# Kernel optimization log

Measured on AMD Instinct MI355X. Metric: run time of the kernel, lower is better.

## Reference

```python
import jax, jax.numpy as jnp
import numpy as np

ALPHA = 0.5
BETA = 0.5


def _attend(qk, feat, W, wp, b):
    """One additive co-attention stage.
    qk:   (B, K)     projected query
    feat: (B, N, D)  keys/values
    W:    (D, K), wp: (2K, 1), b: (N,)
    returns (B, D) attention-weighted sum of feat.
    """
    proj = jnp.einsum('bnd,dk->bnk', feat, W)                    # (B,N,K)
    q = jnp.broadcast_to(qk[:, None, :], proj.shape)             # repeat query
    H = jnp.tanh(jnp.concatenate([q, proj], axis=-1))            # (B,N,2K)
    logits = jnp.einsum('bnk,k->bn', H, wp[:, 0]) + b            # (B,N)
    P = jax.nn.softmax(logits, axis=-1)
    return jnp.einsum('bn,bnd->bd', P, feat)                     # (B,D)


def setup_inputs() -> dict:
    key = jax.random.key(0)
    B, R, S, G, E, D, K = 256, 49, 128, 20, 30, 1024, 256
    ks = jax.random.split(key, 19)
    w = lambda k, shp: 0.05 * jax.random.normal(k, shp, jnp.float32)
    return {
        'ifeature_h': jax.random.normal(ks[0], (B, R, D), jnp.float32),
        'tfeature_h': jax.random.normal(ks[1], (B, S, D), jnp.float32),
        'cfeature':   jax.random.normal(ks[2], (B, G, D), jnp.float32),
        'efeature':   jax.random.normal(ks[3], (B, E, D), jnp.float32),
        'w_Vit_0':  w(ks[4],  (D, K)),
        'w_Vc_0':   w(ks[5],  (D, K)),
        'w_Pc_0':   w(ks[6],  (2 * K, 1)),
        'b_Pc_0':   jnp.zeros((G,), jnp.float32),
        'w_Ve_0':   w(ks[7],  (D, K)),
        'w_Pe_0':   w(ks[8],  (2 * K, 1)),
        'b_Pe_0':   jnp.zeros((E,), jnp.float32),
        'w_Vi_1':   w(ks[9],  (D, K)),
        'w_Vtce_1': w(ks[10], (D, K)),
        'w_Pi_1':   w(ks[11], (2 * K, 1)),
        'b_Pi_1':   jnp.zeros((R,), jnp.float32),
        'w_Vice_2': w(ks[12], (D, K)),
        'w_Vt_2':   w(ks[13], (D, K)),
        'w_Pt_2':   w(ks[14], (2 * K, 1)),
        'b_Pt_2':   jnp.zeros((S,), jnp.float32),
    }


def reference(ifeature_h, tfeature_h, cfeature, efeature,
              w_Vit_0, w_Vc_0, w_Pc_0, b_Pc_0,
              w_Ve_0, w_Pe_0, b_Pe_0,
              w_Vi_1, w_Vtce_1, w_Pi_1, b_Pi_1,
              w_Vice_2, w_Vt_2, w_Pt_2, b_Pt_2):
    ifeat = jnp.mean(ifeature_h, axis=1)   # (B, D)
    tfeat = jnp.mean(tfeature_h, axis=1)   # (B, D)

    # stage 0: image+text query attends over caption group and title
    q0 = (ifeat + tfeat) @ w_Vit_0                               # (B, K)
    Vc = _attend(q0, cfeature, w_Vc_0, w_Pc_0, b_Pc_0)           # (B, D)
    Ve = _attend(q0, efeature, w_Ve_0, w_Pe_0, b_Pe_0)           # (B, D)

    # stage 1: text+caption+title query attends over image regions
    q1 = (tfeat + ALPHA * Vc + BETA * Ve) @ w_Vtce_1
    Vi = _attend(q1, ifeature_h, w_Vi_1, w_Pi_1, b_Pi_1)

    # stage 2: image+caption+title query attends over text tokens
    q2 = (Vi + ALPHA * Vc + BETA * Ve) @ w_Vice_2
    Vt = _attend(q2, tfeature_h, w_Vt_2, w_Pt_2, b_Pt_2)

    return Vi + Vt + ALPHA * Vc + BETA * Ve
```

## Files before the change

kernel.cpp:

```cpp
#include <hip/hip_runtime.h>
#include <hip/hip_bf16.h>
#include <stdint.h>


#define D_DIM 1024
#define K_OUT 256
#define BM 128
#define BK 64
#define NT (D_DIM / BK)

typedef float f32x4 __attribute__((ext_vector_type(4)));
typedef short bf16x8 __attribute__((ext_vector_type(8)));
typedef unsigned short u16x8 __attribute__((ext_vector_type(8)));

static __device__ __forceinline__ unsigned short f2bf(float f) {
    return __builtin_bit_cast(unsigned short, __float2bfloat16(f));
}

static __device__ __forceinline__ float fast_tanh(float x) {
    float e = __expf(2.0f * x);
    return 1.0f - 2.0f / (e + 1.0f);
}

__global__ __launch_bounds__(256) void convert_wt(
    const float* __restrict__ w_c, const float* __restrict__ w_e,
    const float* __restrict__ w_i, const float* __restrict__ w_t,
    unsigned short* __restrict__ wt_all)
{
    const float* wsel[4] = {w_c, w_e, w_i, w_t};
    const float* W = wsel[blockIdx.x];
    unsigned short* Wt = wt_all + (size_t)blockIdx.x * (K_OUT * D_DIM);
    const int d0 = blockIdx.y * 32;

    __shared__ float tile[32][K_OUT];
    const int t = threadIdx.x;
    for (int i = 0; i < 32; ++i) {
        int idx = t + i * 256;
        int dd = idx >> 8, n = idx & 255;
        tile[dd][n] = W[(size_t)(d0 + dd) * K_OUT + n];
    }
    __syncthreads();
    unsigned short buf[32];
#pragma unroll
    for (int dd = 0; dd < 32; ++dd) buf[dd] = f2bf(tile[dd][t]);
#pragma unroll
    for (int i = 0; i < 4; ++i) {
        u16x8 v;
#pragma unroll
        for (int j = 0; j < 8; ++j) v[j] = buf[i * 8 + j];
        *reinterpret_cast<u16x8*>(&Wt[(size_t)t * D_DIM + d0 + i * 8]) = v;
    }
}

struct GemmStage {
    const float* feat;
    const unsigned short* wt;
    const float* wp;
    float* s_out;
    int blk_start;
};

__global__ __launch_bounds__(512) void logits_gemm(
    GemmStage g0, GemmStage g1, GemmStage g2, GemmStage g3)
{
    __shared__ __align__(16) unsigned char AsRaw[BM * 128];
    __shared__ __align__(16) unsigned char WsRaw[K_OUT * 128];
    __shared__ float wp2s[K_OUT];
    __shared__ float partial[BM][4];

    GemmStage st;
    const int bid = blockIdx.x;
    if (bid < g1.blk_start) st = g0;
    else if (bid < g2.blk_start) st = g1;
    else if (bid < g3.blk_start) st = g2;
    else st = g3;
    const int m0 = (bid - st.blk_start) * BM;

    const int t = threadIdx.x;
    if (t < K_OUT) wp2s[t] = st.wp[K_OUT + t];

    const int ar = t >> 2, ac2 = t & 3;
    const int wr = t >> 3, wc = t & 7;
    const int wv = t >> 6, lane = t & 63;
    const int wm = wv >> 2, wn = wv & 3;
    const int q = lane >> 4, c16 = lane & 15;
    const int xa = c16 & 7;

    f32x4 acc[4][4];
#pragma unroll
    for (int i = 0; i < 4; ++i)
#pragma unroll
        for (int j = 0; j < 4; ++j) acc[i][j] = (f32x4){0.f, 0.f, 0.f, 0.f};

    const float* aptr = st.feat + (size_t)(m0 + ar) * D_DIM + ac2 * 16;
    const unsigned short* wptr = st.wt + (size_t)wr * D_DIM + wc * 8;
    const int ab0 = ar * 128 + ((((ac2 * 2)    ) ^ (ar & 7)) << 4);
    const int ab1 = ar * 128 + ((((ac2 * 2) + 1) ^ (ar & 7)) << 4);
    const int wb0 = wr * 128 + ((wc ^ (wr & 7)) << 4);

    f32x4 pa[4];
    u16x8 pw[4];

#pragma unroll
    for (int j = 0; j < 4; ++j) pa[j] = *reinterpret_cast<const f32x4*>(aptr + j * 4);
#pragma unroll
    for (int i = 0; i < 4; ++i) pw[i] = *reinterpret_cast<const u16x8*>(wptr + (size_t)i * 64 * D_DIM);
    {
        u16x8 o0, o1;
#pragma unroll
        for (int j = 0; j < 4; ++j) {
            o0[j] = f2bf(pa[0][j]); o0[4 + j] = f2bf(pa[1][j]);
            o1[j] = f2bf(pa[2][j]); o1[4 + j] = f2bf(pa[3][j]);
        }
        *reinterpret_cast<u16x8*>(&AsRaw[ab0]) = o0;
        *reinterpret_cast<u16x8*>(&AsRaw[ab1]) = o1;
#pragma unroll
        for (int i = 0; i < 4; ++i)
            *reinterpret_cast<u16x8*>(&WsRaw[wb0 + i * 64 * 128]) = pw[i];
    }

#pragma unroll 1
    for (int kt = 0; kt < NT; ++kt) {
        if (kt + 1 < NT) {
            const int d1 = (kt + 1) * BK;
#pragma unroll
            for (int j = 0; j < 4; ++j)
                pa[j] = *reinterpret_cast<const f32x4*>(aptr + d1 + j * 4);
#pragma unroll
            for (int i = 0; i < 4; ++i)
                pw[i] = *reinterpret_cast<const u16x8*>(wptr + (size_t)i * 64 * D_DIM + d1);
        }
        __syncthreads();
#pragma unroll
        for (int ks = 0; ks < 2; ++ks) {
            bf16x8 af[4], bfr[4];
            const int ck = (((ks * 4 + q) ^ xa)) << 4;
#pragma unroll
            for (int mt = 0; mt < 4; ++mt) {
                const int row = wm * 64 + mt * 16 + c16;
                af[mt] = *reinterpret_cast<const bf16x8*>(&AsRaw[row * 128 + ck]);
            }
#pragma unroll
            for (int nt = 0; nt < 4; ++nt) {
                const int row = wn * 64 + nt * 16 + c16;
                bfr[nt] = *reinterpret_cast<const bf16x8*>(&WsRaw[row * 128 + ck]);
            }
#pragma unroll
            for (int mt = 0; mt < 4; ++mt)
#pragma unroll
                for (int nt = 0; nt < 4; ++nt)
                    acc[mt][nt] = __builtin_amdgcn_mfma_f32_16x16x32_bf16(
                        af[mt], bfr[nt], acc[mt][nt], 0, 0, 0);
        }
        __syncthreads();
        if (kt + 1 < NT) {
            u16x8 o0, o1;
#pragma unroll
            for (int j = 0; j < 4; ++j) {
                o0[j] = f2bf(pa[0][j]); o0[4 + j] = f2bf(pa[1][j]);
                o1[j] = f2bf(pa[2][j]); o1[4 + j] = f2bf(pa[3][j]);
            }
            *reinterpret_cast<u16x8*>(&AsRaw[ab0]) = o0;
            *reinterpret_cast<u16x8*>(&AsRaw[ab1]) = o1;
#pragma unroll
            for (int i = 0; i < 4; ++i)
                *reinterpret_cast<u16x8*>(&WsRaw[wb0 + i * 64 * 128]) = pw[i];
        }
    }

#pragma unroll
    for (int mt = 0; mt < 4; ++mt) {
#pragma unroll
        for (int r = 0; r < 4; ++r) {
            float v = 0.f;
#pragma unroll
            for (int nt = 0; nt < 4; ++nt) {
                const int col = wn * 64 + nt * 16 + c16;
                v += fast_tanh(acc[mt][nt][r]) * wp2s[col];
            }
            v += __shfl_xor(v, 1);
            v += __shfl_xor(v, 2);
            v += __shfl_xor(v, 4);
            v += __shfl_xor(v, 8);
            if (c16 == 0) partial[wm * 64 + mt * 16 + q * 4 + r][wn] = v;
        }
    }
    __syncthreads();
    if (t < BM)
        st.s_out[m0 + t] = partial[t][0] + partial[t][1] + partial[t][2] + partial[t][3];
}

struct PVStage {
    const float* s;
    const float* bias;
    const float* feat;
    float* v_out;
    int N;
};

__global__ __launch_bounds__(256) void softmax_pv(
    PVStage p0, PVStage p1, PVStage p2, PVStage p3)
{
    PVStage st = (blockIdx.y == 0) ? p0 : (blockIdx.y == 1) ? p1
               : (blockIdx.y == 2) ? p2 : p3;
    const int b = blockIdx.x, t = threadIdx.x;
    const int N = st.N;

    __shared__ float P[128];
    __shared__ float inv_s;

    if (t < N) P[t] = st.s[b * N + t] + st.bias[t];
    __syncthreads();
    if (t < 64) {
        float m = -3.4e38f;
        for (int n = t; n < N; n += 64) m = fmaxf(m, P[n]);
#pragma unroll
        for (int sh = 32; sh; sh >>= 1) m = fmaxf(m, __shfl_xor(m, sh));
        float ssum = 0.f;
        for (int n = t; n < N; n += 64) { float e = __expf(P[n] - m); P[n] = e; ssum += e; }
#pragma unroll
        for (int sh = 32; sh; sh >>= 1) ssum += __shfl_xor(ssum, sh);
        if (t == 0) inv_s = 1.0f / ssum;
    }
    __syncthreads();
    const float inv = inv_s;

    f32x4 accv = (f32x4){0.f, 0.f, 0.f, 0.f};
    const float* fb = st.feat + (size_t)b * N * D_DIM + t * 4;
    for (int n = 0; n < N; ++n) {
        f32x4 f = *reinterpret_cast<const f32x4*>(fb + (size_t)n * D_DIM);
        accv += (P[n] * inv) * f;
    }
    *reinterpret_cast<f32x4*>(&st.v_out[(size_t)b * D_DIM + t * 4]) = accv;
}

__global__ __launch_bounds__(256) void combine_out(
    const float* __restrict__ vc, const float* __restrict__ ve,
    const float* __restrict__ vi, const float* __restrict__ vt,
    float* __restrict__ out)
{
    const int i = (blockIdx.x * 256 + threadIdx.x) * 4;
    f32x4 a = *reinterpret_cast<const f32x4*>(vi + i);
    f32x4 bb = *reinterpret_cast<const f32x4*>(vt + i);
    f32x4 c = *reinterpret_cast<const f32x4*>(vc + i);
    f32x4 e = *reinterpret_cast<const f32x4*>(ve + i);
    *reinterpret_cast<f32x4*>(out + i) = a + bb + 0.5f * c + 0.5f * e;
}

extern "C" void kernel_launch(void* const* d_in, const int* in_sizes, int n_in,
                              void* d_out, int out_size, void* d_ws, size_t ws_size,
                              hipStream_t stream)
{
    const float* ifeature = (const float*)d_in[0];
    const float* tfeature = (const float*)d_in[1];
    const float* cfeature = (const float*)d_in[2];
    const float* efeature = (const float*)d_in[3];
    const float* w_Vc = (const float*)d_in[5];
    const float* w_Pc = (const float*)d_in[6];
    const float* b_Pc = (const float*)d_in[7];
    const float* w_Ve = (const float*)d_in[8];
    const float* w_Pe = (const float*)d_in[9];
    const float* b_Pe = (const float*)d_in[10];
    const float* w_Vi = (const float*)d_in[11];
    const float* w_Pi = (const float*)d_in[13];
    const float* b_Pi = (const float*)d_in[14];
    const float* w_Vt = (const float*)d_in[16];
    const float* w_Pt = (const float*)d_in[17];
    const float* b_Pt = (const float*)d_in[18];

    char* ws = (char*)d_ws;
    unsigned short* wt = (unsigned short*)ws;
    float* s_c = (float*)(ws + 2u * 1024 * 1024);
    float* s_e = s_c + 5120;
    float* s_i = s_e + 7680;
    float* s_t = s_i + 12544;
    float* v_c = (float*)(ws + 3u * 1024 * 1024);
    float* v_e = v_c + 256 * 1024;
    float* v_i = v_e + 256 * 1024;
    float* v_t = v_i + 256 * 1024;

    convert_wt<<<dim3(4, 32), 256, 0, stream>>>(w_Vc, w_Ve, w_Vi, w_Vt, wt);

    GemmStage g0{cfeature, wt + 0 * (K_OUT * D_DIM), w_Pc, s_c, 0};
    GemmStage g1{efeature, wt + 1 * (K_OUT * D_DIM), w_Pe, s_e, 40};
    GemmStage g2{ifeature, wt + 2 * (K_OUT * D_DIM), w_Pi, s_i, 100};
    GemmStage g3{tfeature, wt + 3 * (K_OUT * D_DIM), w_Pt, s_t, 198};
    logits_gemm<<<454, 512, 0, stream>>>(g0, g1, g2, g3);

    PVStage p0{s_c, b_Pc, cfeature, v_c, 20};
    PVStage p1{s_e, b_Pe, efeature, v_e, 30};
    PVStage p2{s_i, b_Pi, ifeature, v_i, 49};
    PVStage p3{s_t, b_Pt, tfeature, v_t, 128};
    softmax_pv<<<dim3(256, 4), 256, 0, stream>>>(p0, p1, p2, p3);

    combine_out<<<256, 256, 0, stream>>>(v_c, v_e, v_i, v_t, (float*)d_out);
}
```

Before: 113.4 us.

## Pre-swizzle bf16 weights into MFMA fragment layout and read B directly from global

```diff
diff --git a/kernel.cpp b/kernel.cpp
--- a/kernel.cpp
+++ b/kernel.cpp
@@ -5,9 +5,9 @@
 
 #define D_DIM 1024
 #define K_OUT 256
-#define BM 128
+#define BM 64
 #define BK 64
-#define NT (D_DIM / BK)
+#define NT 16
 
 typedef float f32x4 __attribute__((ext_vector_type(4)));
 typedef short bf16x8 __attribute__((ext_vector_type(8)));
@@ -25,31 +25,25 @@
 __global__ __launch_bounds__(256) void convert_wt(
     const float* __restrict__ w_c, const float* __restrict__ w_e,
     const float* __restrict__ w_i, const float* __restrict__ w_t,
-    unsigned short* __restrict__ wt_all)
+    unsigned short* __restrict__ wtf)
 {
     const float* wsel[4] = {w_c, w_e, w_i, w_t};
     const float* W = wsel[blockIdx.x];
-    unsigned short* Wt = wt_all + (size_t)blockIdx.x * (K_OUT * D_DIM);
-    const int d0 = blockIdx.y * 32;
-
-    __shared__ float tile[32][K_OUT];
+    unsigned short* out = wtf + (size_t)blockIdx.x * (K_OUT * D_DIM);
+    const int kb = blockIdx.y;
     const int t = threadIdx.x;
-    for (int i = 0; i < 32; ++i) {
-        int idx = t + i * 256;
-        int dd = idx >> 8, n = idx & 255;
-        tile[dd][n] = W[(size_t)(d0 + dd) * K_OUT + n];
-    }
-    __syncthreads();
-    unsigned short buf[32];
-#pragma unroll
-    for (int dd = 0; dd < 32; ++dd) buf[dd] = f2bf(tile[dd][t]);
-#pragma unroll
-    for (int i = 0; i < 4; ++i) {
-        u16x8 v;
-#pragma unroll
-        for (int j = 0; j < 8; ++j) v[j] = buf[i * 8 + j];
-        *reinterpret_cast<u16x8*>(&Wt[(size_t)t * D_DIM + d0 + i * 8]) = v;
-    }
+
+    unsigned short tmp[16];
+#pragma unroll
+    for (int j = 0; j < 16; ++j)
+        tmp[j] = f2bf(W[(size_t)(kb * 16 + j) * K_OUT + t]);
+
+    u16x8 lo, hi;
+#pragma unroll
+    for (int j = 0; j < 8; ++j) { lo[j] = tmp[j]; hi[j] = tmp[8 + j]; }
+    unsigned short* dst = out + (size_t)kb * 4096 + t * 16;
+    *reinterpret_cast<u16x8*>(dst) = lo;
+    *reinterpret_cast<u16x8*>(dst + 8) = hi;
 }
 
 struct GemmStage {
@@ -60,16 +54,14 @@
     int blk_start;
 };
 
-__global__ __launch_bounds__(512) void logits_gemm(
+__global__ __launch_bounds__(256, 3) void logits_gemm(
     GemmStage g0, GemmStage g1, GemmStage g2, GemmStage g3)
 {
-    __shared__ __align__(16) unsigned char AsRaw[BM * 128];
-    __shared__ __align__(16) unsigned char WsRaw[K_OUT * 128];
-    __shared__ float wp2s[K_OUT];
+    __shared__ __align__(16) unsigned char As[2][BM * 128];
     __shared__ float partial[BM][4];
 
+    const int bid = blockIdx.x;
     GemmStage st;
-    const int bid = blockIdx.x;
     if (bid < g1.blk_start) st = g0;
     else if (bid < g2.blk_start) st = g1;
     else if (bid < g3.blk_start) st = g2;
@@ -77,14 +69,21 @@
     const int m0 = (bid - st.blk_start) * BM;
 
     const int t = threadIdx.x;
-    if (t < K_OUT) wp2s[t] = st.wp[K_OUT + t];
-
-    const int ar = t >> 2, ac2 = t & 3;
-    const int wr = t >> 3, wc = t & 7;
+    const int r = t >> 2, qd = t & 3;
     const int wv = t >> 6, lane = t & 63;
-    const int wm = wv >> 2, wn = wv & 3;
     const int q = lane >> 4, c16 = lane & 15;
-    const int xa = c16 & 7;
+
+    const float* aptr = st.feat + (size_t)(m0 + r) * D_DIM + qd * 16;
+    const int wo0 = r * 128 + (((qd * 2    ) ^ (r & 7)) << 4);
+    const int wo1 = r * 128 + (((qd * 2 + 1) ^ (r & 7)) << 4);
+    const unsigned short* bb = st.wt + (q >> 1) * 4096
+                             + ((wv * 64 + c16) << 4) + (q & 1) * 8;
+    const int ck0 = ((0 * 4 + q) ^ (c16 & 7)) << 4;
+    const int ck1 = ((1 * 4 + q) ^ (c16 & 7)) << 4;
+
+    float wpf[4];
+#pragma unroll
+    for (int nt = 0; nt < 4; ++nt) wpf[nt] = st.wp[K_OUT + wv * 64 + nt * 16 + c16];
 
     f32x4 acc[4][4];
 #pragma unroll
@@ -92,19 +91,10 @@
 #pragma unroll
         for (int j = 0; j < 4; ++j) acc[i][j] = (f32x4){0.f, 0.f, 0.f, 0.f};
 
-    const float* aptr = st.feat + (size_t)(m0 + ar) * D_DIM + ac2 * 16;
-    const unsigned short* wptr = st.wt + (size_t)wr * D_DIM + wc * 8;
-    const int ab0 = ar * 128 + ((((ac2 * 2)    ) ^ (ar & 7)) << 4);
-    const int ab1 = ar * 128 + ((((ac2 * 2) + 1) ^ (ar & 7)) << 4);
-    const int wb0 = wr * 128 + ((wc ^ (wr & 7)) << 4);
-
     f32x4 pa[4];
-    u16x8 pw[4];
-
-#pragma unroll
-    for (int j = 0; j < 4; ++j) pa[j] = *reinterpret_cast<const f32x4*>(aptr + j * 4);
-#pragma unroll
-    for (int i = 0; i < 4; ++i) pw[i] = *reinterpret_cast<const u16x8*>(wptr + (size_t)i * 64 * D_DIM);
+#pragma unroll
+    for (int j = 0; j < 4; ++j)
+        pa[j] = *reinterpret_cast<const f32x4*>(aptr + j * 4);
     {
         u16x8 o0, o1;
 #pragma unroll
@@ -112,47 +102,40 @@
             o0[j] = f2bf(pa[0][j]); o0[4 + j] = f2bf(pa[1][j]);
             o1[j] = f2bf(pa[2][j]); o1[4 + j] = f2bf(pa[3][j]);
         }
-        *reinterpret_cast<u16x8*>(&AsRaw[ab0]) = o0;
-        *reinterpret_cast<u16x8*>(&AsRaw[ab1]) = o1;
-#pragma unroll
-        for (int i = 0; i < 4; ++i)
-            *reinterpret_cast<u16x8*>(&WsRaw[wb0 + i * 64 * 128]) = pw[i];
+        *reinterpret_cast<u16x8*>(&As[0][wo0]) = o0;
+        *reinterpret_cast<u16x8*>(&As[0][wo1]) = o1;
     }
 
 #pragma unroll 1
     for (int kt = 0; kt < NT; ++kt) {
-        if (kt + 1 < NT) {
-            const int d1 = (kt + 1) * BK;
-#pragma unroll
-            for (int j = 0; j < 4; ++j)
-                pa[j] = *reinterpret_cast<const f32x4*>(aptr + d1 + j * 4);
-#pragma unroll
-            for (int i = 0; i < 4; ++i)
-                pw[i] = *reinterpret_cast<const u16x8*>(wptr + (size_t)i * 64 * D_DIM + d1);
-        }
         __syncthreads();
+        u16x8 bfr[2][4];
+        const unsigned short* bk = bb + kt * 16384;
+#pragma unroll
+        for (int ks = 0; ks < 2; ++ks)
+#pragma unroll
+            for (int nt = 0; nt < 4; ++nt)
+                bfr[ks][nt] = *reinterpret_cast<const u16x8*>(bk + ks * 8192 + nt * 256);
+        const int ktn = (kt + 1) & 15;
+#pragma unroll
+        for (int j = 0; j < 4; ++j)
+            pa[j] = *reinterpret_cast<const f32x4*>(aptr + ktn * 64 + j * 4);
+        const unsigned char* buf = As[kt & 1];
 #pragma unroll
         for (int ks = 0; ks < 2; ++ks) {
-            bf16x8 af[4], bfr[4];
-            const int ck = (((ks * 4 + q) ^ xa)) << 4;
-#pragma unroll
-            for (int mt = 0; mt < 4; ++mt) {
-                const int row = wm * 64 + mt * 16 + c16;
-                af[mt] = *reinterpret_cast<const bf16x8*>(&AsRaw[row * 128 + ck]);
-            }
-#pragma unroll
-            for (int nt = 0; nt < 4; ++nt) {
-                const int row = wn * 64 + nt * 16 + c16;
-                bfr[nt] = *reinterpret_cast<const bf16x8*>(&WsRaw[row * 128 + ck]);
-            }
+            const int ck = ks ? ck1 : ck0;
+            bf16x8 af[4];
+#pragma unroll
+            for (int mt = 0; mt < 4; ++mt)
+                af[mt] = *reinterpret_cast<const bf16x8*>(&buf[(mt * 16 + c16) * 128 + ck]);
 #pragma unroll
             for (int mt = 0; mt < 4; ++mt)
 #pragma unroll
                 for (int nt = 0; nt < 4; ++nt)
                     acc[mt][nt] = __builtin_amdgcn_mfma_f32_16x16x32_bf16(
-                        af[mt], bfr[nt], acc[mt][nt], 0, 0, 0);
-        }
-        __syncthreads();
+                        af[mt], __builtin_bit_cast(bf16x8, bfr[ks][nt]),
+                        acc[mt][nt], 0, 0, 0);
+        }
         if (kt + 1 < NT) {
             u16x8 o0, o1;
 #pragma unroll
@@ -160,29 +143,25 @@
                 o0[j] = f2bf(pa[0][j]); o0[4 + j] = f2bf(pa[1][j]);
                 o1[j] = f2bf(pa[2][j]); o1[4 + j] = f2bf(pa[3][j]);
             }
-            *reinterpret_cast<u16x8*>(&AsRaw[ab0]) = o0;
-            *reinterpret_cast<u16x8*>(&AsRaw[ab1]) = o1;
-#pragma unroll
-            for (int i = 0; i < 4; ++i)
-                *reinterpret_cast<u16x8*>(&WsRaw[wb0 + i * 64 * 128]) = pw[i];
+            unsigned char* nbuf = As[(kt + 1) & 1];
+            *reinterpret_cast<u16x8*>(&nbuf[wo0]) = o0;
+            *reinterpret_cast<u16x8*>(&nbuf[wo1]) = o1;
         }
     }
 
 #pragma unroll
     for (int mt = 0; mt < 4; ++mt) {
 #pragma unroll
-        for (int r = 0; r < 4; ++r) {
+        for (int rg = 0; rg < 4; ++rg) {
             float v = 0.f;
 #pragma unroll
-            for (int nt = 0; nt < 4; ++nt) {
-                const int col = wn * 64 + nt * 16 + c16;
-                v += fast_tanh(acc[mt][nt][r]) * wp2s[col];
-            }
+            for (int nt = 0; nt < 4; ++nt)
+                v += fast_tanh(acc[mt][nt][rg]) * wpf[nt];
             v += __shfl_xor(v, 1);
             v += __shfl_xor(v, 2);
             v += __shfl_xor(v, 4);
             v += __shfl_xor(v, 8);
-            if (c16 == 0) partial[wm * 64 + mt * 16 + q * 4 + r][wn] = v;
+            if (c16 == 0) partial[mt * 16 + q * 4 + rg][wv] = v;
         }
     }
     __syncthreads();
@@ -269,7 +248,7 @@
     const float* b_Pt = (const float*)d_in[18];
 
     char* ws = (char*)d_ws;
-    unsigned short* wt = (unsigned short*)ws;
+    unsigned short* wtf = (unsigned short*)ws;
     float* s_c = (float*)(ws + 2u * 1024 * 1024);
     float* s_e = s_c + 5120;
     float* s_i = s_e + 7680;
@@ -279,13 +258,13 @@
     float* v_i = v_e + 256 * 1024;
     float* v_t = v_i + 256 * 1024;
 
-    convert_wt<<<dim3(4, 32), 256, 0, stream>>>(w_Vc, w_Ve, w_Vi, w_Vt, wt);
-
-    GemmStage g0{cfeature, wt + 0 * (K_OUT * D_DIM), w_Pc, s_c, 0};
-    GemmStage g1{efeature, wt + 1 * (K_OUT * D_DIM), w_Pe, s_e, 40};
-    GemmStage g2{ifeature, wt + 2 * (K_OUT * D_DIM), w_Pi, s_i, 100};
-    GemmStage g3{tfeature, wt + 3 * (K_OUT * D_DIM), w_Pt, s_t, 198};
-    logits_gemm<<<454, 512, 0, stream>>>(g0, g1, g2, g3);
+    convert_wt<<<dim3(4, 64), 256, 0, stream>>>(w_Vc, w_Ve, w_Vi, w_Vt, wtf);
+
+    GemmStage g0{cfeature, wtf,          w_Pc, s_c, 0};
+    GemmStage g1{efeature, wtf + 262144, w_Pe, s_e, 80};
+    GemmStage g2{ifeature, wtf + 524288, w_Pi, s_i, 200};
+    GemmStage g3{tfeature, wtf + 786432, w_Pt, s_t, 396};
+    logits_gemm<<<908, 256, 0, stream>>>(g0, g1, g2, g3);
 
     PVStage p0{s_c, b_Pc, cfeature, v_c, 20};
     PVStage p1{s_e, b_Pe, efeature, v_e, 30};
```

Result: faster. 99.38 us (-12.4%).
